# Kernel tuning notes

Hardware: AMD Instinct MI355X
Metric: run time of the kernel (lower is better)

Reference implementation:

```python
import jax, jax.numpy as jnp
import numpy as np

N_NODES = 89250


def gcn_conv(x, W, b, src, dst, n):
    # h = X W  (dense transform before aggregation, as in PyG GCNConv)
    h = x @ W
    # add self loops
    loop = jnp.arange(n, dtype=src.dtype)
    src_all = jnp.concatenate([src, loop])
    dst_all = jnp.concatenate([dst, loop])
    # symmetric degree normalization D^-1/2 A_hat D^-1/2 (degree from targets)
    deg = jax.ops.segment_sum(jnp.ones_like(dst_all, dtype=h.dtype), dst_all, num_segments=n)
    dinv = jnp.where(deg > 0, jax.lax.rsqrt(deg), 0.0)
    norm = dinv[src_all] * dinv[dst_all]  # [E+n]
    # gather source features, scale, scatter-add to targets
    msg = h[src_all] * norm[:, None]
    out = jax.ops.segment_sum(msg, dst_all, num_segments=n)
    return out + b


def setup_inputs() -> dict:
    key = jax.random.key(0)
    k1, k2, k3, k4, k5 = jax.random.split(key, 5)
    n, f, h, c, e = N_NODES, 500, 64, 7, 899756
    x = jax.random.normal(k1, (n, f), dtype=jnp.float32)
    edge_index = jax.random.randint(k2, (2, e), 0, n, dtype=jnp.int64)
    W1 = jax.random.normal(k3, (f, h), dtype=jnp.float32) / np.sqrt(f)
    b1 = jnp.zeros((h,), dtype=jnp.float32)
    W2 = jax.random.normal(k4, (h, c), dtype=jnp.float32) / np.sqrt(h)
    b2 = jnp.zeros((c,), dtype=jnp.float32)
    return {"x": x, "W1": W1, "b1": b1, "W2": W2, "b2": b2, "edge_index": edge_index}


def reference(x, W1, b1, W2, b2, edge_index):
    n = x.shape[0]
    src, dst = edge_index[0], edge_index[1]
    h = jax.nn.relu(gcn_conv(x, W1, b1, src, dst, n))
    out = gcn_conv(h, W2, b2, src, dst, n)
    return out
```

## Files before the change

### kernel.cpp

```cpp
#include <hip/hip_runtime.h>
#include <cstdint>

#define F_IN 500
#define HID  64
#define NCLS 7

typedef __attribute__((ext_vector_type(8))) short v8s;
typedef __attribute__((ext_vector_type(4))) short v4s;
typedef __attribute__((ext_vector_type(4))) float v4f;

union S8 { v8s v; v4s h[2]; };

static inline size_t align_up(size_t v, size_t a) { return (v + a - 1) & ~(a - 1); }

__device__ inline unsigned short f2bf(float f) {
    unsigned int u = __float_as_uint(f);
    u += 0x7FFF + ((u >> 16) & 1);
    return (unsigned short)(u >> 16);
}

__global__ void hist_kernel(const int* __restrict__ dst, int* __restrict__ hist, int E) {
    int i = blockIdx.x * blockDim.x + threadIdx.x;
    if (i < E) atomicAdd(&hist[dst[i]], 1);
}

__global__ void dinv_kernel(const int* __restrict__ hist, float* __restrict__ dinv, int n) {
    int i = blockIdx.x * blockDim.x + threadIdx.x;
    if (i < n) dinv[i] = rsqrtf((float)hist[i] + 1.0f);
}

__global__ __launch_bounds__(256) void scan1_kernel(const int* __restrict__ hist,
                                                    int* __restrict__ rowstart,
                                                    int* __restrict__ bsum, int n) {
    __shared__ int sdat[256];
    int tid = threadIdx.x;
    int i = blockIdx.x * 256 + tid;
    int v = (i < n) ? hist[i] : 0;
    sdat[tid] = v;
    __syncthreads();
    for (int off = 1; off < 256; off <<= 1) {
        int t = (tid >= off) ? sdat[tid - off] : 0;
        __syncthreads();
        sdat[tid] += t;
        __syncthreads();
    }
    int incl = sdat[tid];
    if (i < n) rowstart[i] = incl - v;
    if (tid == 255) bsum[blockIdx.x] = incl;
}

__global__ __launch_bounds__(512) void scan2_kernel(int* __restrict__ bsum, int nb) {
    __shared__ int sdat[512];
    int tid = threadIdx.x;
    int v = (tid < nb) ? bsum[tid] : 0;
    sdat[tid] = v;
    __syncthreads();
    for (int off = 1; off < 512; off <<= 1) {
        int t = (tid >= off) ? sdat[tid - off] : 0;
        __syncthreads();
        sdat[tid] += t;
        __syncthreads();
    }
    bsum[tid] = sdat[tid] - v;
}

__global__ void scan3_kernel(int* __restrict__ rowstart, const int* __restrict__ bsum,
                             int* __restrict__ cursor, int n, int E) {
    int i = blockIdx.x * blockDim.x + threadIdx.x;
    if (i < n) {
        int val = rowstart[i] + bsum[i >> 8];
        rowstart[i] = val;
        cursor[i] = val;
    }
    if (i == 0) rowstart[n] = E;
}

__global__ void scatter_kernel(const int* __restrict__ src, const int* __restrict__ dst,
                               int* __restrict__ cursor, int* __restrict__ csrc, int E) {
    int e = blockIdx.x * blockDim.x + threadIdx.x;
    if (e < E) {
        int d = dst[e];
        int pos = atomicAdd(&cursor[d], 1);
        csrc[pos] = src[e];
    }
}

__global__ void wt_kernel(const float* __restrict__ W1, unsigned short* __restrict__ Wt) {
    int id = blockIdx.x * 256 + threadIdx.x;
    if (id >= HID * 512) return;
    int c = id >> 9;
    int k = id & 511;
    Wt[(size_t)c * 512 + k] = (k < F_IN) ? f2bf(W1[(size_t)k * HID + c]) : (unsigned short)0;
}

__global__ __launch_bounds__(256) void gemm1_mfma_kernel(
    const float* __restrict__ x, const unsigned short* __restrict__ Wt,
    float* __restrict__ h0, int n)
{
    __shared__ unsigned short Al[128][36];
    __shared__ unsigned short Bl[64][36];

    const int tid  = threadIdx.x;
    const int lane = tid & 63;
    const int wave = tid >> 6;
    const int row0 = blockIdx.x * 128;
    const int l15  = lane & 15;
    const int kq   = (lane >> 4) * 4;

    v4f acc[2][4];
    #pragma unroll
    for (int rb = 0; rb < 2; ++rb)
        #pragma unroll
        for (int cb = 0; cb < 4; ++cb) acc[rb][cb] = (v4f)(0.0f);

    const int a_c4 = tid & 7;
    const int a_r  = tid >> 3;
    const int b_c  = tid >> 2;
    const int b_k8 = (tid & 3) * 8;

    for (int ks = 0; ks < 16; ++ks) {
        const int kbase = ks * 32;
        __syncthreads();
        #pragma unroll
        for (int i = 0; i < 4; ++i) {
            const int r = a_r + 32 * i;
            int row = row0 + r;
            row = (row < n) ? row : (n - 1);
            v4s o;
            if (kbase + a_c4 * 4 < F_IN) {
                float4 v = *reinterpret_cast<const float4*>(
                    x + (size_t)row * F_IN + kbase + a_c4 * 4);
                o.x = (short)f2bf(v.x); o.y = (short)f2bf(v.y);
                o.z = (short)f2bf(v.z); o.w = (short)f2bf(v.w);
            } else {
                o = (v4s)(short)0;
            }
            *reinterpret_cast<v4s*>(&Al[r][a_c4 * 4]) = o;
        }
        {
            const unsigned short* p = Wt + (size_t)b_c * 512 + kbase + b_k8;
            v4s lo = *reinterpret_cast<const v4s*>(p);
            v4s hi = *reinterpret_cast<const v4s*>(p + 4);
            *reinterpret_cast<v4s*>(&Bl[b_c][b_k8])     = lo;
            *reinterpret_cast<v4s*>(&Bl[b_c][b_k8 + 4]) = hi;
        }
        __syncthreads();

        S8 af[2], bq[4];
        #pragma unroll
        for (int rb = 0; rb < 2; ++rb) {
            const int row = wave * 32 + rb * 16 + l15;
            af[rb].h[0] = *reinterpret_cast<const v4s*>(&Al[row][kq]);
            af[rb].h[1] = *reinterpret_cast<const v4s*>(&Al[row][kq + 16]);
        }
        #pragma unroll
        for (int cb = 0; cb < 4; ++cb) {
            const int col = cb * 16 + l15;
            bq[cb].h[0] = *reinterpret_cast<const v4s*>(&Bl[col][kq]);
            bq[cb].h[1] = *reinterpret_cast<const v4s*>(&Bl[col][kq + 16]);
        }
        #pragma unroll
        for (int rb = 0; rb < 2; ++rb)
            #pragma unroll
            for (int cb = 0; cb < 4; ++cb)
                acc[rb][cb] = __builtin_amdgcn_mfma_f32_16x16x32_bf16(
                    af[rb].v, bq[cb].v, acc[rb][cb], 0, 0, 0);
    }

    #pragma unroll
    for (int rb = 0; rb < 2; ++rb) {
        #pragma unroll
        for (int cb = 0; cb < 4; ++cb) {
            #pragma unroll
            for (int j = 0; j < 4; ++j) {
                int row = row0 + wave * 32 + rb * 16 + (lane >> 4) * 4 + j;
                if (row < n)
                    h0[(size_t)row * HID + cb * 16 + l15] = acc[rb][cb][j];
            }
        }
    }
}

__global__ __launch_bounds__(256) void agg1_gemm2_kernel(
    const float* __restrict__ h0, const float* __restrict__ dinv,
    const int* __restrict__ rowstart, const int* __restrict__ csrc,
    const float* __restrict__ b1, const float* __restrict__ W2,
    float* __restrict__ h2, int n)
{
    __shared__ float W2s[HID][9];
    __shared__ float b1s[HID];
    for (int i = threadIdx.x; i < HID * 8; i += 256) {
        int k = i >> 3, c = i & 7;
        W2s[k][c] = (c < NCLS) ? W2[k * NCLS + c] : 0.f;
    }
    if (threadIdx.x < HID) b1s[threadIdx.x] = b1[threadIdx.x];
    __syncthreads();

    const int lane = threadIdx.x & 63;
    const int wave = threadIdx.x >> 6;
    const int d = blockIdx.x * 4 + wave;
    if (d >= n) return;

    const int js = rowstart[d];
    const int je = rowstart[d + 1];
    float acc = 0.f;
    for (int j = js; j < je; ++j) {
        int s = csrc[j];
        acc = fmaf(h0[(size_t)s * HID + lane], dinv[s], acc);
    }
    const float dd = dinv[d];
    float v = (acc + dd * h0[(size_t)d * HID + lane]) * dd;
    float p = fmaxf(v + b1s[lane], 0.f);

    float t0 = p * W2s[lane][0];
    float t1 = p * W2s[lane][1];
    float t2 = p * W2s[lane][2];
    float t3 = p * W2s[lane][3];
    float t4 = p * W2s[lane][4];
    float t5 = p * W2s[lane][5];
    float t6 = p * W2s[lane][6];
    #pragma unroll
    for (int off = 32; off > 0; off >>= 1) {
        t0 += __shfl_xor(t0, off);
        t1 += __shfl_xor(t1, off);
        t2 += __shfl_xor(t2, off);
        t3 += __shfl_xor(t3, off);
        t4 += __shfl_xor(t4, off);
        t5 += __shfl_xor(t5, off);
        t6 += __shfl_xor(t6, off);
    }
    float sel = t0;
    sel = (lane == 1) ? t1 : sel;
    sel = (lane == 2) ? t2 : sel;
    sel = (lane == 3) ? t3 : sel;
    sel = (lane == 4) ? t4 : sel;
    sel = (lane == 5) ? t5 : sel;
    sel = (lane == 6) ? t6 : sel;
    if (lane < NCLS) h2[(size_t)d * 8 + lane] = sel;
}

__global__ void agg2_kernel(const float* __restrict__ h2, const float* __restrict__ dinv,
                            const int* __restrict__ rowstart, const int* __restrict__ csrc,
                            const float* __restrict__ b2, float* __restrict__ out, int n)
{
    int idx = blockIdx.x * blockDim.x + threadIdx.x;
    int d = idx >> 3;
    int c = idx & 7;
    if (d >= n) return;

    const int js = rowstart[d];
    const int je = rowstart[d + 1];
    float acc = 0.f;
    for (int j = js; j < je; ++j) {
        int s = csrc[j];
        acc = fmaf(h2[(size_t)s * 8 + c], dinv[s], acc);
    }
    const float dd = dinv[d];
    if (c < NCLS)
        out[(size_t)d * NCLS + c] = fmaf(acc + dd * h2[(size_t)d * 8 + c], dd, b2[c]);
}

extern "C" void kernel_launch(void* const* d_in, const int* in_sizes, int n_in,
                              void* d_out, int out_size, void* d_ws, size_t ws_size,
                              hipStream_t stream)
{
    const float* x  = (const float*)d_in[0];
    const float* W1 = (const float*)d_in[1];
    const float* b1 = (const float*)d_in[2];
    const float* W2 = (const float*)d_in[3];
    const float* b2 = (const float*)d_in[4];
    const int*   ei = (const int*)d_in[5];

    const int n = in_sizes[0] / F_IN;
    const int E = in_sizes[5] / 2;
    const int* src = ei;
    const int* dst = ei + E;

    char* ws = (char*)d_ws;
    size_t off = 0;
    int*   hist     = (int*)(ws + off);   off += align_up((size_t)n * 4, 256);
    int*   rowstart = (int*)(ws + off);   off += align_up((size_t)(n + 1) * 4, 256);
    int*   bsum     = (int*)(ws + off);   off += align_up((size_t)512 * 4, 256);
    int*   csrc     = (int*)(ws + off);   off += align_up((size_t)E * 4, 256);
    float* dinv     = (float*)(ws + off); off += align_up((size_t)n * 4, 256);
    float* h0       = (float*)(ws + off); off += align_up((size_t)n * HID * 4, 256);
    float* h2       = (float*)(ws + off); off += align_up((size_t)n * 8 * 4, 256);
    unsigned short* Wt = (unsigned short*)(ws + off); off += align_up((size_t)HID * 512 * 2, 256);
    float* out      = (float*)d_out;

    const int nb = (n + 255) / 256;

    hipMemsetAsync(hist, 0, (size_t)n * 4, stream);
    hist_kernel<<<(E + 255) / 256, 256, 0, stream>>>(dst, hist, E);
    dinv_kernel<<<nb, 256, 0, stream>>>(hist, dinv, n);
    scan1_kernel<<<nb, 256, 0, stream>>>(hist, rowstart, bsum, n);
    scan2_kernel<<<1, 512, 0, stream>>>(bsum, nb);
    scan3_kernel<<<nb, 256, 0, stream>>>(rowstart, bsum, hist , n, E);
    scatter_kernel<<<(E + 255) / 256, 256, 0, stream>>>(src, dst, hist , csrc, E);

    wt_kernel<<<(HID * 512 + 255) / 256, 256, 0, stream>>>(W1, Wt);
    gemm1_mfma_kernel<<<(n + 127) / 128, 256, 0, stream>>>(x, Wt, h0, n);

    agg1_gemm2_kernel<<<(n + 3) / 4, 256, 0, stream>>>(h0, dinv, rowstart, csrc, b1, W2, h2, n);

    agg2_kernel<<<((size_t)n * 8 + 255) / 256, 256, 0, stream>>>(h2, dinv, rowstart, csrc, b2, out, n);
}
```

Measured before the change: 503.9 us.

## Prescale features by source dinv, store h0 in bf16, unroll gathers

Folds the source-side degree normalization into the producers: gemm1 multiplies each row by dinv and writes h0 as bf16, and agg1 writes h2 already scaled by dinv. The aggregation loops therefore drop the per-edge dinv[s] gather and sum plain values, unrolled by four for memory-level parallelism. The dinv computation is merged into the scan1 kernel, removing one launch. Storing h0 in bf16 halves the gather traffic but adds rounding error to the hidden features.

```diff
diff --git a/kernel.cpp b/kernel.cpp
--- a/kernel.cpp
+++ b/kernel.cpp
@@ -18,24 +18,24 @@
     u += 0x7FFF + ((u >> 16) & 1);
     return (unsigned short)(u >> 16);
 }
+__device__ inline float bf2f(unsigned short u) {
+    return __uint_as_float(((unsigned int)u) << 16);
+}
 
 __global__ void hist_kernel(const int* __restrict__ dst, int* __restrict__ hist, int E) {
     int i = blockIdx.x * blockDim.x + threadIdx.x;
     if (i < E) atomicAdd(&hist[dst[i]], 1);
 }
 
-__global__ void dinv_kernel(const int* __restrict__ hist, float* __restrict__ dinv, int n) {
-    int i = blockIdx.x * blockDim.x + threadIdx.x;
-    if (i < n) dinv[i] = rsqrtf((float)hist[i] + 1.0f);
-}
-
 __global__ __launch_bounds__(256) void scan1_kernel(const int* __restrict__ hist,
                                                     int* __restrict__ rowstart,
-                                                    int* __restrict__ bsum, int n) {
+                                                    int* __restrict__ bsum,
+                                                    float* __restrict__ dinv, int n) {
     __shared__ int sdat[256];
     int tid = threadIdx.x;
     int i = blockIdx.x * 256 + tid;
     int v = (i < n) ? hist[i] : 0;
+    if (i < n) dinv[i] = rsqrtf((float)v + 1.0f);
     sdat[tid] = v;
     __syncthreads();
     for (int off = 1; off < 256; off <<= 1) {
@@ -95,7 +95,8 @@
 
 __global__ __launch_bounds__(256) void gemm1_mfma_kernel(
     const float* __restrict__ x, const unsigned short* __restrict__ Wt,
-    float* __restrict__ h0, int n)
+    const float* __restrict__ dinv,
+    unsigned short* __restrict__ h0s, int n)
 {
     __shared__ unsigned short Al[128][36];
     __shared__ unsigned short Bl[64][36];
@@ -170,22 +171,23 @@
     #pragma unroll
     for (int rb = 0; rb < 2; ++rb) {
         #pragma unroll
-        for (int cb = 0; cb < 4; ++cb) {
-            #pragma unroll
-            for (int j = 0; j < 4; ++j) {
-                int row = row0 + wave * 32 + rb * 16 + (lane >> 4) * 4 + j;
-                if (row < n)
-                    h0[(size_t)row * HID + cb * 16 + l15] = acc[rb][cb][j];
+        for (int j = 0; j < 4; ++j) {
+            int row = row0 + wave * 32 + rb * 16 + (lane >> 4) * 4 + j;
+            if (row < n) {
+                float di = dinv[row];
+                #pragma unroll
+                for (int cb = 0; cb < 4; ++cb)
+                    h0s[(size_t)row * HID + cb * 16 + l15] = f2bf(acc[rb][cb][j] * di);
             }
         }
     }
 }
 
 __global__ __launch_bounds__(256) void agg1_gemm2_kernel(
-    const float* __restrict__ h0, const float* __restrict__ dinv,
+    const unsigned short* __restrict__ h0s, const float* __restrict__ dinv,
     const int* __restrict__ rowstart, const int* __restrict__ csrc,
     const float* __restrict__ b1, const float* __restrict__ W2,
-    float* __restrict__ h2, int n)
+    float* __restrict__ h2s, int n)
 {
     __shared__ float W2s[HID][9];
     __shared__ float b1s[HID];
@@ -204,13 +206,24 @@
     const int js = rowstart[d];
     const int je = rowstart[d + 1];
     float acc = 0.f;
-    for (int j = js; j < je; ++j) {
-        int s = csrc[j];
-        acc = fmaf(h0[(size_t)s * HID + lane], dinv[s], acc);
-    }
+    int j = js;
+    for (; j + 4 <= je; j += 4) {
+        int s0 = csrc[j + 0];
+        int s1 = csrc[j + 1];
+        int s2 = csrc[j + 2];
+        int s3 = csrc[j + 3];
+        float v0 = bf2f(h0s[(size_t)s0 * HID + lane]);
+        float v1 = bf2f(h0s[(size_t)s1 * HID + lane]);
+        float v2 = bf2f(h0s[(size_t)s2 * HID + lane]);
+        float v3 = bf2f(h0s[(size_t)s3 * HID + lane]);
+        acc += (v0 + v1) + (v2 + v3);
+    }
+    for (; j < je; ++j)
+        acc += bf2f(h0s[(size_t)csrc[j] * HID + lane]);
+    acc += bf2f(h0s[(size_t)d * HID + lane]);
+
     const float dd = dinv[d];
-    float v = (acc + dd * h0[(size_t)d * HID + lane]) * dd;
-    float p = fmaxf(v + b1s[lane], 0.f);
+    float p = fmaxf(acc * dd + b1s[lane], 0.f);
 
     float t0 = p * W2s[lane][0];
     float t1 = p * W2s[lane][1];
@@ -236,10 +249,10 @@
     sel = (lane == 4) ? t4 : sel;
     sel = (lane == 5) ? t5 : sel;
     sel = (lane == 6) ? t6 : sel;
-    if (lane < NCLS) h2[(size_t)d * 8 + lane] = sel;
-}
-
-__global__ void agg2_kernel(const float* __restrict__ h2, const float* __restrict__ dinv,
+    if (lane < NCLS) h2s[(size_t)d * 8 + lane] = sel * dd;
+}
+
+__global__ void agg2_kernel(const float* __restrict__ h2s, const float* __restrict__ dinv,
                             const int* __restrict__ rowstart, const int* __restrict__ csrc,
                             const float* __restrict__ b2, float* __restrict__ out, int n)
 {
@@ -251,13 +264,24 @@
     const int js = rowstart[d];
     const int je = rowstart[d + 1];
     float acc = 0.f;
-    for (int j = js; j < je; ++j) {
-        int s = csrc[j];
-        acc = fmaf(h2[(size_t)s * 8 + c], dinv[s], acc);
-    }
-    const float dd = dinv[d];
+    int j = js;
+    for (; j + 4 <= je; j += 4) {
+        int s0 = csrc[j + 0];
+        int s1 = csrc[j + 1];
+        int s2 = csrc[j + 2];
+        int s3 = csrc[j + 3];
+        float v0 = h2s[(size_t)s0 * 8 + c];
+        float v1 = h2s[(size_t)s1 * 8 + c];
+        float v2 = h2s[(size_t)s2 * 8 + c];
+        float v3 = h2s[(size_t)s3 * 8 + c];
+        acc += (v0 + v1) + (v2 + v3);
+    }
+    for (; j < je; ++j)
+        acc += h2s[(size_t)csrc[j] * 8 + c];
+    acc += h2s[(size_t)d * 8 + c];
+
     if (c < NCLS)
-        out[(size_t)d * NCLS + c] = fmaf(acc + dd * h2[(size_t)d * 8 + c], dd, b2[c]);
+        out[(size_t)d * NCLS + c] = fmaf(acc, dinv[d], b2[c]);
 }
 
 extern "C" void kernel_launch(void* const* d_in, const int* in_sizes, int n_in,
@@ -283,8 +307,8 @@
     int*   bsum     = (int*)(ws + off);   off += align_up((size_t)512 * 4, 256);
     int*   csrc     = (int*)(ws + off);   off += align_up((size_t)E * 4, 256);
     float* dinv     = (float*)(ws + off); off += align_up((size_t)n * 4, 256);
-    float* h0       = (float*)(ws + off); off += align_up((size_t)n * HID * 4, 256);
-    float* h2       = (float*)(ws + off); off += align_up((size_t)n * 8 * 4, 256);
+    unsigned short* h0s = (unsigned short*)(ws + off); off += align_up((size_t)n * HID * 2, 256);
+    float* h2s      = (float*)(ws + off); off += align_up((size_t)n * 8 * 4, 256);
     unsigned short* Wt = (unsigned short*)(ws + off); off += align_up((size_t)HID * 512 * 2, 256);
     float* out      = (float*)d_out;
 
@@ -292,16 +316,15 @@
 
     hipMemsetAsync(hist, 0, (size_t)n * 4, stream);
     hist_kernel<<<(E + 255) / 256, 256, 0, stream>>>(dst, hist, E);
-    dinv_kernel<<<nb, 256, 0, stream>>>(hist, dinv, n);
-    scan1_kernel<<<nb, 256, 0, stream>>>(hist, rowstart, bsum, n);
+    scan1_kernel<<<nb, 256, 0, stream>>>(hist, rowstart, bsum, dinv, n);
     scan2_kernel<<<1, 512, 0, stream>>>(bsum, nb);
     scan3_kernel<<<nb, 256, 0, stream>>>(rowstart, bsum, hist , n, E);
     scatter_kernel<<<(E + 255) / 256, 256, 0, stream>>>(src, dst, hist , csrc, E);
 
     wt_kernel<<<(HID * 512 + 255) / 256, 256, 0, stream>>>(W1, Wt);
-    gemm1_mfma_kernel<<<(n + 127) / 128, 256, 0, stream>>>(x, Wt, h0, n);
-
-    agg1_gemm2_kernel<<<(n + 3) / 4, 256, 0, stream>>>(h0, dinv, rowstart, csrc, b1, W2, h2, n);
-
-    agg2_kernel<<<((size_t)n * 8 + 255) / 256, 256, 0, stream>>>(h2, dinv, rowstart, csrc, b2, out, n);
-}
+    gemm1_mfma_kernel<<<(n + 127) / 128, 256, 0, stream>>>(x, Wt, dinv, h0s, n);
+
+    agg1_gemm2_kernel<<<(n + 3) / 4, 256, 0, stream>>>(h0s, dinv, rowstart, csrc, b1, W2, h2s, n);
+
+    agg2_kernel<<<((size_t)n * 8 + 255) / 256, 256, 0, stream>>>(h2s, dinv, rowstart, csrc, b2, out, n);
+}
```

Result: faster. 453.5 us (-10.0%).
